# Optimization experiments

Hardware: AMD Instinct MI355X
Metric: run time of the kernel (lower is better)

Reference implementation:

```python
import jax, jax.numpy as jnp
import numpy as np

N, E, F, H, C = 100000, 3200000, 128, 256, 47
EPS = 1e-5


def setup_inputs() -> dict:
    key = jax.random.key(0)
    ks = jax.random.split(key, 12)
    x = jax.random.normal(ks[0], (N, F), dtype=jnp.float32)
    edge_index = jax.random.randint(ks[1], (2, E), 0, N, dtype=jnp.int64)
    relations = jax.random.randint(ks[2], (E,), 0, 4, dtype=jnp.int64)
    def lin(k, fan_in, fan_out):
        return jax.random.normal(k, (fan_in, fan_out), dtype=jnp.float32) / np.sqrt(fan_in)
    W0 = lin(ks[3], F, H); b0 = jnp.zeros((H,), jnp.float32)
    W1 = lin(ks[4], H, H); b1 = jnp.zeros((H,), jnp.float32)
    W2 = lin(ks[5], H, C); b2 = jnp.zeros((C,), jnp.float32)
    g0 = jnp.ones((H,), jnp.float32); be0 = jnp.zeros((H,), jnp.float32)
    g1 = jnp.ones((H,), jnp.float32); be1 = jnp.zeros((H,), jnp.float32)
    return {"x": x, "edge_index": edge_index, "relations": relations,
            "W0": W0, "b0": b0, "g0": g0, "be0": be0,
            "W1": W1, "b1": b1, "g1": g1, "be1": be1,
            "W2": W2, "b2": b2}


def _gcn_conv(x, W, b, src, dst, n_nodes):
    # GCNConv: linear transform, add self-loops, symmetric degree normalization,
    # gather-scale-scatter aggregation, bias add.
    h = x @ W  # [N, out]
    self_loop = jnp.arange(n_nodes, dtype=src.dtype)
    s = jnp.concatenate([src, self_loop])
    d = jnp.concatenate([dst, self_loop])
    deg = jax.ops.segment_sum(jnp.ones(d.shape[0], h.dtype), d, num_segments=n_nodes)
    dinv = jnp.where(deg > 0, jax.lax.rsqrt(deg), 0.0)
    coef = dinv[s] * dinv[d]  # [E+N]
    out = jax.ops.segment_sum(h[s] * coef[:, None], d, num_segments=n_nodes)
    return out + b


def _batch_norm(x, gamma, beta):
    mean = jnp.mean(x, axis=0)
    var = jnp.var(x, axis=0)
    return (x - mean) * jax.lax.rsqrt(var + EPS) * gamma + beta


def reference(x, edge_index, relations, W0, b0, g0, be0, W1, b1, g1, be1, W2, b2):
    src, dst = edge_index[0], edge_index[1]
    n = x.shape[0]
    h = _gcn_conv(x, W0, b0, src, dst, n)
    h = jax.nn.relu(_batch_norm(h, g0, be0))  # dropout is identity in eval
    h = _gcn_conv(h, W1, b1, src, dst, n)
    h = jax.nn.relu(_batch_norm(h, g1, be1))
    h = _gcn_conv(h, W2, b2, src, dst, n)
    return jax.nn.log_softmax(h, axis=-1)
```

## Files before the change

### kernel.cpp

```cpp
#include <hip/hip_runtime.h>
#include <hip/hip_fp8.h>
#include <math.h>

#define NN 100000
#define NE 3200000
#define FIN 128
#define HD 256
#define CO 47
#define NBKT 196
#define G 1024
#define CHUNK 3125

typedef _Float16 h2 __attribute__((ext_vector_type(2)));
typedef _Float16 h4 __attribute__((ext_vector_type(4)));
typedef _Float16 h8 __attribute__((ext_vector_type(8)));
typedef float f32x2 __attribute__((ext_vector_type(2)));
typedef float f32x4 __attribute__((ext_vector_type(4)));
typedef unsigned int u32x2 __attribute__((ext_vector_type(2)));
typedef unsigned int u32x4 __attribute__((ext_vector_type(4)));


__global__ __launch_bounds__(256) void hist_kernel(const int* __restrict__ dst,
                                                   int* __restrict__ hist) {
    __shared__ int h[NBKT];
    int tid = threadIdx.x;
    for (int i = tid; i < NBKT; i += 256) h[i] = 0;
    __syncthreads();
    int base = blockIdx.x * CHUNK;
    for (int i = tid; i < CHUNK; i += 256)
        atomicAdd(&h[dst[base + i] >> 9], 1);
    __syncthreads();
    for (int i = tid; i < NBKT; i += 256) hist[i * G + blockIdx.x] = h[i];
}

__global__ __launch_bounds__(256) void rowscan_kernel(int* __restrict__ hist,
                                                      int* __restrict__ btot) {
    __shared__ int sums[256];
    int b = blockIdx.x, t = threadIdx.x;
    int base = b * G + t * 4;
    int4 v = *(int4*)&hist[base];
    int i0 = v.x, i1 = i0 + v.y, i2 = i1 + v.z, i3 = i2 + v.w;
    sums[t] = i3;
    __syncthreads();
    #pragma unroll
    for (int off = 1; off < 256; off <<= 1) {
        int u = (t >= off) ? sums[t - off] : 0;
        __syncthreads();
        sums[t] += u;
        __syncthreads();
    }
    int excl = sums[t] - i3;
    hist[base] = excl;
    hist[base + 1] = excl + i0;
    hist[base + 2] = excl + i1;
    hist[base + 3] = excl + i2;
    if (t == 255) btot[b] = sums[255];
}

__global__ void totscan_kernel(const int* __restrict__ btot, int* __restrict__ bbase) {
    __shared__ int tmp[256];
    int t = threadIdx.x;
    int v = (t < NBKT) ? btot[t] : 0;
    tmp[t] = v;
    __syncthreads();
    #pragma unroll
    for (int off = 1; off < 256; off <<= 1) {
        int u = (t >= off) ? tmp[t - off] : 0;
        __syncthreads();
        tmp[t] += u;
        __syncthreads();
    }
    if (t < NBKT) bbase[t] = tmp[t] - v;
    if (t == NBKT - 1) bbase[NBKT] = tmp[t];
}

__global__ __launch_bounds__(256) void scatter_kernel(const int* __restrict__ src,
                                                      const int* __restrict__ dst,
                                                      const int* __restrict__ hscan,
                                                      const int* __restrict__ bbase,
                                                      int* __restrict__ epk) {
    __shared__ int cur[NBKT];
    int tid = threadIdx.x;
    for (int i = tid; i < NBKT; i += 256)
        cur[i] = hscan[i * G + blockIdx.x] + bbase[i];
    __syncthreads();
    int base = blockIdx.x * CHUNK;
    for (int i = tid; i < CHUNK; i += 256) {
        int e = base + i;
        int d = dst[e];
        int slot = atomicAdd(&cur[d >> 9], 1);
        epk[slot] = ((d & 511) << 17) | src[e];
    }
}

__global__ __launch_bounds__(256) void bucket_fill_kernel(
    const int* __restrict__ bbase, const int* __restrict__ epk,
    int* __restrict__ csr, int* __restrict__ offs, float* __restrict__ dinv)
{
    __shared__ int deg[512], cur[512], a0[512], a1[512];
    int tid = threadIdx.x, b = blockIdx.x;
    int ebeg = bbase[b], eend = bbase[b + 1];
    deg[tid] = 0; deg[tid + 256] = 0;
    __syncthreads();
    for (int e = ebeg + tid; e < eend; e += 256)
        atomicAdd(&deg[((unsigned)epk[e]) >> 17], 1);
    __syncthreads();
    a0[tid] = deg[tid]; a0[tid + 256] = deg[tid + 256];
    __syncthreads();
    int* pin = a0; int* pout = a1;
    for (int off = 1; off < 512; off <<= 1) {
        #pragma unroll
        for (int q = 0; q < 2; ++q) {
            int p = tid + q * 256;
            pout[p] = pin[p] + ((p >= off) ? pin[p - off] : 0);
        }
        __syncthreads();
        int* t = pin; pin = pout; pout = t;
    }
    #pragma unroll
    for (int q = 0; q < 2; ++q) {
        int i = tid + q * 256;
        int excl = pin[i] - deg[i];
        cur[i] = excl;
        int node = b * 512 + i;
        if (node < NN) {
            offs[node] = ebeg + excl;
            dinv[node] = rsqrtf((float)deg[i] + 1.0f);
        }
    }
    if (b == 0 && tid == 0) offs[NN] = NE;
    __syncthreads();
    for (int e = ebeg + tid; e < eend; e += 256) {
        int pk = epk[e];
        int p = atomicAdd(&cur[((unsigned)pk) >> 17], 1);
        csr[ebeg + p] = pk & 0x1FFFF;
    }
}


__global__ void wtrans_all_kernel(const float* __restrict__ W0,
                                  const float* __restrict__ W1,
                                  const float* __restrict__ W2,
                                  _Float16* __restrict__ wt0,
                                  _Float16* __restrict__ wt1,
                                  _Float16* __restrict__ wt2) {
    int i = blockIdx.x * 256 + threadIdx.x;
    if (i < 256 * 128) {
        int n = i >> 7, k = i & 127;
        wt0[i] = (_Float16)W0[k * 256 + n];
    } else if (i < 256 * 128 + 256 * 256) {
        int t = i - 256 * 128;
        int n = t >> 8, k = t & 255;
        wt1[t] = (_Float16)W1[k * 256 + n];
    } else if (i < 256 * 128 + 256 * 256 + 64 * 256) {
        int t = i - 256 * 128 - 256 * 256;
        int n = t >> 8, k = t & 255;
        wt2[t] = (_Float16)((n < CO) ? W2[k * CO + n] : 0.0f);
    }
}


__global__ void conv_x_kernel(const float* __restrict__ x, const float* __restrict__ dinv,
                              unsigned* __restrict__ xq) {
    int i = blockIdx.x * 256 + threadIdx.x;
    if (i >= NN * FIN / 4) return;
    int r = i >> 5;
    float4 v = ((const float4*)x)[i];
    float dv = dinv[r];
    int u = __builtin_amdgcn_cvt_pk_fp8_f32(v.x * dv, v.y * dv, 0, false);
    u = __builtin_amdgcn_cvt_pk_fp8_f32(v.z * dv, v.w * dv, u, true);
    xq[i] = (unsigned)u;
}


__global__ __launch_bounds__(256) void agg128_kernel(
    const unsigned* __restrict__ xq, const int* __restrict__ offs,
    const int* __restrict__ csr, const float* __restrict__ dinv,
    _Float16* __restrict__ out)
{
    int lane = threadIdx.x & 63;
    int grp = lane >> 5;
    int gl = lane & 31;
    int v = blockIdx.x * 4 + (threadIdx.x >> 6);
    f32x2 a01 = {0.f, 0.f}, a23 = {0.f, 0.f};
    if (grp == 0) {
        unsigned sv = xq[(size_t)v * 32 + gl];
        a01 += __builtin_amdgcn_cvt_pk_f32_fp8((int)sv, false);
        a23 += __builtin_amdgcn_cvt_pk_f32_fp8((int)sv, true);
    }
    int b = offs[v], e = offs[v + 1];
    int j = b + grp;
    int s[8];
    bool have = (j + 14 < e);
    if (have) {
        #pragma unroll
        for (int q = 0; q < 8; ++q) s[q] = csr[j + 2 * q];
    }
    while (have) {
        int nj = j + 16;
        bool nhave = (nj + 14 < e);
        int ns[8];
        if (nhave) {
            #pragma unroll
            for (int q = 0; q < 8; ++q) ns[q] = csr[nj + 2 * q];
        }
        #pragma unroll
        for (int q = 0; q < 8; ++q) {
            unsigned t = xq[(size_t)s[q] * 32 + gl];
            a01 += __builtin_amdgcn_cvt_pk_f32_fp8((int)t, false);
            a23 += __builtin_amdgcn_cvt_pk_f32_fp8((int)t, true);
        }
        #pragma unroll
        for (int q = 0; q < 8; ++q) s[q] = ns[q];
        j = nj; have = nhave;
    }
    for (; j < e; j += 2) {
        unsigned t = xq[(size_t)csr[j] * 32 + gl];
        a01 += __builtin_amdgcn_cvt_pk_f32_fp8((int)t, false);
        a23 += __builtin_amdgcn_cvt_pk_f32_fp8((int)t, true);
    }
    a01[0] += __shfl_xor(a01[0], 32, 64);
    a01[1] += __shfl_xor(a01[1], 32, 64);
    a23[0] += __shfl_xor(a23[0], 32, 64);
    a23[1] += __shfl_xor(a23[1], 32, 64);
    if (grp == 0) {
        float dv = dinv[v];
        h4 o; o[0] = (_Float16)(a01[0] * dv); o[1] = (_Float16)(a01[1] * dv);
        o[2] = (_Float16)(a23[0] * dv); o[3] = (_Float16)(a23[1] * dv);
        ((h4*)out)[(size_t)v * 32 + gl] = o;
    }
}

__global__ __launch_bounds__(256) void agg256_kernel(
    const unsigned* __restrict__ t1q, const int* __restrict__ offs,
    const int* __restrict__ csr, const float* __restrict__ dinv,
    unsigned* __restrict__ out)
{
    int lane = threadIdx.x & 63;
    int v = blockIdx.x * 4 + (threadIdx.x >> 6);
    unsigned sv = t1q[(size_t)v * 64 + lane];
    f32x2 acc01 = __builtin_amdgcn_cvt_pk_f32_fp8((int)sv, false);
    f32x2 acc23 = __builtin_amdgcn_cvt_pk_f32_fp8((int)sv, true);
    int b = offs[v], e = offs[v + 1], j = b;
    int s[8];
    if (j + 8 <= e) {
        #pragma unroll
        for (int q = 0; q < 8; ++q) s[q] = csr[j + q];
    }
    for (; j + 8 <= e; ) {
        int nj = j + 8;
        int ns[8];
        if (nj + 8 <= e) {
            #pragma unroll
            for (int q = 0; q < 8; ++q) ns[q] = csr[nj + q];
        }
        #pragma unroll
        for (int q = 0; q < 8; ++q) {
            unsigned t = t1q[(size_t)s[q] * 64 + lane];
            acc01 += __builtin_amdgcn_cvt_pk_f32_fp8((int)t, false);
            acc23 += __builtin_amdgcn_cvt_pk_f32_fp8((int)t, true);
        }
        #pragma unroll
        for (int q = 0; q < 8; ++q) s[q] = ns[q];
        j = nj;
    }
    for (; j < e; ++j) {
        unsigned t = t1q[(size_t)csr[j] * 64 + lane];
        acc01 += __builtin_amdgcn_cvt_pk_f32_fp8((int)t, false);
        acc23 += __builtin_amdgcn_cvt_pk_f32_fp8((int)t, true);
    }
    float dv = dinv[v];
    int pk = __builtin_amdgcn_cvt_pk_fp8_f32(acc01[0] * dv, acc01[1] * dv, 0, false);
    pk = __builtin_amdgcn_cvt_pk_fp8_f32(acc23[0] * dv, acc23[1] * dv, pk, true);
    out[(size_t)v * 64 + lane] = (unsigned)pk;
}

__global__ __launch_bounds__(256) void agg47_lsm_kernel(
    const unsigned* __restrict__ t2q, const int* __restrict__ offs,
    const int* __restrict__ csr, const float* __restrict__ dinv,
    const float* __restrict__ bias, float* __restrict__ out)
{
    int lane = threadIdx.x & 63;
    int grp = lane >> 4;
    int gl = lane & 15;
    int v = blockIdx.x * 4 + (threadIdx.x >> 6);
    f32x2 a01 = {0.f, 0.f}, a23 = {0.f, 0.f};
    if (grp == 0) {
        unsigned u = t2q[(size_t)v * 16 + gl];
        a01 += __builtin_amdgcn_cvt_pk_f32_fp8((int)u, false);
        a23 += __builtin_amdgcn_cvt_pk_f32_fp8((int)u, true);
    }
    int b = offs[v], e = offs[v + 1];
    int j = b + grp;
    int s[8];
    bool have = (j + 28 < e);
    if (have) {
        #pragma unroll
        for (int q = 0; q < 8; ++q) s[q] = csr[j + 4 * q];
    }
    while (have) {
        int nj = j + 32;
        bool nhave = (nj + 28 < e);
        int ns[8];
        if (nhave) {
            #pragma unroll
            for (int q = 0; q < 8; ++q) ns[q] = csr[nj + 4 * q];
        }
        #pragma unroll
        for (int q = 0; q < 8; ++q) {
            unsigned t = t2q[(size_t)s[q] * 16 + gl];
            a01 += __builtin_amdgcn_cvt_pk_f32_fp8((int)t, false);
            a23 += __builtin_amdgcn_cvt_pk_f32_fp8((int)t, true);
        }
        #pragma unroll
        for (int q = 0; q < 8; ++q) s[q] = ns[q];
        j = nj; have = nhave;
    }
    for (; j < e; j += 4) {
        unsigned t = t2q[(size_t)csr[j] * 16 + gl];
        a01 += __builtin_amdgcn_cvt_pk_f32_fp8((int)t, false);
        a23 += __builtin_amdgcn_cvt_pk_f32_fp8((int)t, true);
    }
    #pragma unroll
    for (int o = 16; o <= 32; o <<= 1) {
        a01[0] += __shfl_xor(a01[0], o, 64);
        a01[1] += __shfl_xor(a01[1], o, 64);
        a23[0] += __shfl_xor(a23[0], o, 64);
        a23[1] += __shfl_xor(a23[1], o, 64);
    }
    float dv = dinv[v];
    float vals[4] = {a01[0], a01[1], a23[0], a23[1]};
    float vv[4];
    #pragma unroll
    for (int k = 0; k < 4; ++k) {
        int c = 4 * gl + k;
        vv[k] = (c < CO) ? fmaf(vals[k], dv, bias[c]) : -1e30f;
    }
    float m = fmaxf(fmaxf(vv[0], vv[1]), fmaxf(vv[2], vv[3]));
    #pragma unroll
    for (int o = 8; o > 0; o >>= 1) m = fmaxf(m, __shfl_xor(m, o, 64));
    float sum = 0.f;
    #pragma unroll
    for (int k = 0; k < 4; ++k) sum += (vv[k] > -1e29f) ? expf(vv[k] - m) : 0.f;
    #pragma unroll
    for (int o = 8; o > 0; o >>= 1) sum += __shfl_xor(sum, o, 64);
    float lse = m + logf(sum);
    if (grp == 0) {
        #pragma unroll
        for (int k = 0; k < 4; ++k) {
            int c = 4 * gl + k;
            if (c < CO) out[(size_t)v * CO + c] = vv[k] - lse;
        }
    }
}


#define LDS_PAD 8

template<int K, bool XFORM, bool EPI_DINV, bool OUT8, bool BNSTAT>
__global__ __launch_bounds__(256) void mfma_gemm_big(
    const _Float16* __restrict__ A, int lda,
    const _Float16* __restrict__ Wt,
    const float* __restrict__ ss, const float* __restrict__ dinv,
    void* __restrict__ outp, int ldo, float* __restrict__ part8)
{
    __shared__ __align__(16) _Float16 As[128][64 + LDS_PAD];
    __shared__ __align__(16) _Float16 Bs[128][64 + LDS_PAD];
    __shared__ float SS[2 * K];
    __shared__ float cstat[256];
    const int row0 = (blockIdx.x >> 1) * 128;
    const int col0 = (blockIdx.x & 1) * 128;
    const int tid = threadIdx.x;
    if (XFORM) {
        for (int i = tid; i < 2 * K; i += 256) SS[i] = ss[i];
    }
    if (BNSTAT) cstat[tid] = 0.f;
    const int lane = tid & 63;
    const int wv = tid >> 6;
    const int wr = wv >> 1, wc = wv & 1;
    const int fr = lane & 15;
    const int kb = (lane >> 4) * 8;

    f32x4 acc[4][4];
    #pragma unroll
    for (int m = 0; m < 4; ++m)
        #pragma unroll
        for (int n = 0; n < 4; ++n)
            acc[m][n] = (f32x4){0.f, 0.f, 0.f, 0.f};

    if (XFORM || BNSTAT) __syncthreads();

    for (int k0 = 0; k0 < K; k0 += 64) {
        #pragma unroll
        for (int p = 0; p < 4; ++p) {
            int c = p * 256 + tid;
            int m = c >> 3, kk = (c & 7) * 8;
            int r = row0 + m;
            h8 av = {};
            if (r < NN) av = *(const h8*)&A[(size_t)r * lda + k0 + kk];
            if (XFORM) {
                #pragma unroll
                for (int j = 0; j < 8; ++j) {
                    float a = (float)av[j];
                    a = fmaxf(fmaf(a, SS[k0 + kk + j], SS[K + k0 + kk + j]), 0.0f);
                    av[j] = (_Float16)a;
                }
            }
            *(h8*)&As[m][kk] = av;
        }
        #pragma unroll
        for (int p = 0; p < 4; ++p) {
            int c = p * 256 + tid;
            int n = c >> 3, kk = (c & 7) * 8;
            h8 bv = *(const h8*)&Wt[(size_t)(col0 + n) * K + k0 + kk];
            *(h8*)&Bs[n][kk] = bv;
        }
        __syncthreads();
        #pragma unroll
        for (int ks = 0; ks < 2; ++ks) {
            h8 a[4], b[4];
            #pragma unroll
            for (int m = 0; m < 4; ++m)
                a[m] = *(const h8*)&As[wr * 64 + m * 16 + fr][ks * 32 + kb];
            #pragma unroll
            for (int n = 0; n < 4; ++n)
                b[n] = *(const h8*)&Bs[wc * 64 + n * 16 + fr][ks * 32 + kb];
            #pragma unroll
            for (int m = 0; m < 4; ++m)
                #pragma unroll
                for (int n = 0; n < 4; ++n)
                    acc[m][n] = __builtin_amdgcn_mfma_f32_16x16x32_f16(a[m], b[n], acc[m][n], 0, 0, 0);
        }
        __syncthreads();
    }

    const int fq = lane >> 4;
    if (OUT8) {
        unsigned char* stg = (unsigned char*)&As[0][0];
        #pragma unroll
        for (int m = 0; m < 4; ++m) {
            #pragma unroll
            for (int j = 0; j < 4; ++j) {
                int rr = wr * 64 + m * 16 + fq * 4 + j;
                int r = row0 + rr;
                float dv = (EPI_DINV && r < NN) ? dinv[r] : 1.0f;
                #pragma unroll
                for (int n = 0; n < 4; n += 2) {
                    int cc0 = wc * 64 + n * 16 + fr;
                    float v0 = acc[m][n][j] * dv;
                    float v1 = acc[m][n + 1][j] * dv;
                    int pk = __builtin_amdgcn_cvt_pk_fp8_f32(v0, v1, 0, false);
                    stg[rr * 128 + cc0] = (unsigned char)(pk & 0xFF);
                    stg[rr * 128 + cc0 + 16] = (unsigned char)((pk >> 8) & 0xFF);
                }
            }
        }
        __syncthreads();
        #pragma unroll
        for (int p = 0; p < 4; ++p) {
            int rr = p * 32 + (tid >> 3);
            int cc = (tid & 7) * 16;
            int r = row0 + rr;
            if (r < NN)
                *(u32x4*)&((unsigned char*)outp)[(size_t)r * ldo + col0 + cc] =
                    *(u32x4*)&stg[rr * 128 + cc];
        }
    } else {
        float ps[4] = {}, pq[4] = {};
        #pragma unroll
        for (int m = 0; m < 4; ++m) {
            #pragma unroll
            for (int j = 0; j < 4; ++j) {
                int r = row0 + wr * 64 + m * 16 + fq * 4 + j;
                if (r >= NN) continue;
                float dv = EPI_DINV ? dinv[r] : 1.0f;
                #pragma unroll
                for (int n = 0; n < 4; ++n) {
                    int c = col0 + wc * 64 + n * 16 + fr;
                    float val = acc[m][n][j] * dv;
                    ((_Float16*)outp)[(size_t)r * ldo + c] = (_Float16)val;
                    if (BNSTAT) { ps[n] += val; pq[n] += val * val; }
                }
            }
        }
        if (BNSTAT) {
            #pragma unroll
            for (int n = 0; n < 4; ++n) {
                int cc = wc * 64 + n * 16 + fr;
                atomicAdd(&cstat[cc], ps[n]);
                atomicAdd(&cstat[128 + cc], pq[n]);
            }
            __syncthreads();
            if (tid < 128) {
                int rep = (blockIdx.x & 7) * 512;
                atomicAdd(&part8[rep + col0 + tid], cstat[tid]);
                atomicAdd(&part8[rep + 256 + col0 + tid], cstat[128 + tid]);
            }
        }
    }
}


__global__ __launch_bounds__(256) void mfma_gemm2_kernel(
    const unsigned* __restrict__ Aq,
    const _Float16* __restrict__ Wt,
    const float* __restrict__ ss, const float* __restrict__ dinv,
    unsigned char* __restrict__ t2q)
{
    __shared__ __align__(16) _Float16 As[128][32 + LDS_PAD];
    __shared__ __align__(16) _Float16 Bs[64][32 + LDS_PAD];
    __shared__ float SS[2 * HD];
    const int row0 = blockIdx.x * 128;
    const int tid = threadIdx.x;
    for (int i = tid; i < 2 * HD; i += 256) SS[i] = ss[i];
    const int lane = tid & 63;
    const int wv = tid >> 6;
    const int wr = wv >> 1, wc = wv & 1;
    const int fr = lane & 15;
    const int kb = (lane >> 4) * 8;

    f32x4 acc[4][2];
    #pragma unroll
    for (int m = 0; m < 4; ++m)
        #pragma unroll
        for (int n = 0; n < 2; ++n)
            acc[m][n] = (f32x4){0.f, 0.f, 0.f, 0.f};

    __syncthreads();

    for (int k0 = 0; k0 < HD; k0 += 32) {
        #pragma unroll
        for (int p = 0; p < 2; ++p) {
            int idx = (p * 256 + tid) * 8;
            int m = idx >> 5, kk = idx & 31;
            int r = row0 + m;
            float vals[8] = {};
            if (r < NN) {
                u32x2 u = *(const u32x2*)&Aq[(size_t)r * 64 + ((k0 + kk) >> 2)];
                f32x2 p0 = __builtin_amdgcn_cvt_pk_f32_fp8((int)u[0], false);
                f32x2 p1 = __builtin_amdgcn_cvt_pk_f32_fp8((int)u[0], true);
                f32x2 p2 = __builtin_amdgcn_cvt_pk_f32_fp8((int)u[1], false);
                f32x2 p3 = __builtin_amdgcn_cvt_pk_f32_fp8((int)u[1], true);
                vals[0] = p0[0]; vals[1] = p0[1]; vals[2] = p1[0]; vals[3] = p1[1];
                vals[4] = p2[0]; vals[5] = p2[1]; vals[6] = p3[0]; vals[7] = p3[1];
            }
            h8 av;
            #pragma unroll
            for (int j = 0; j < 8; ++j) {
                float a = fmaxf(fmaf(vals[j], SS[k0 + kk + j], SS[HD + k0 + kk + j]), 0.0f);
                av[j] = (_Float16)a;
            }
            *(h8*)&As[m][kk] = av;
        }
        {
            int idx = tid * 8;
            int n = idx >> 5, kk = idx & 31;
            h8 bv = *(const h8*)&Wt[(size_t)n * HD + k0 + kk];
            *(h8*)&Bs[n][kk] = bv;
        }
        __syncthreads();
        h8 a[4], b[2];
        #pragma unroll
        for (int m = 0; m < 4; ++m)
            a[m] = *(const h8*)&As[wr * 64 + m * 16 + fr][kb];
        #pragma unroll
        for (int n = 0; n < 2; ++n)
            b[n] = *(const h8*)&Bs[wc * 32 + n * 16 + fr][kb];
        #pragma unroll
        for (int m = 0; m < 4; ++m)
            #pragma unroll
            for (int n = 0; n < 2; ++n)
                acc[m][n] = __builtin_amdgcn_mfma_f32_16x16x32_f16(a[m], b[n], acc[m][n], 0, 0, 0);
        __syncthreads();
    }

    const int fq = lane >> 4;
    unsigned char* stg = (unsigned char*)&As[0][0];
    #pragma unroll
    for (int m = 0; m < 4; ++m) {
        #pragma unroll
        for (int j = 0; j < 4; ++j) {
            int rr = wr * 64 + m * 16 + fq * 4 + j;
            int r = row0 + rr;
            float dv = (r < NN) ? dinv[r] : 1.0f;
            int cc0 = wc * 32 + fr;
            float v0 = acc[m][0][j] * dv;
            float v1 = acc[m][1][j] * dv;
            int pk = __builtin_amdgcn_cvt_pk_fp8_f32(v0, v1, 0, false);
            stg[rr * 64 + cc0] = (unsigned char)(pk & 0xFF);
            stg[rr * 64 + cc0 + 16] = (unsigned char)((pk >> 8) & 0xFF);
        }
    }
    __syncthreads();
    #pragma unroll
    for (int p = 0; p < 2; ++p) {
        int idx = p * 256 + tid;
        int rr = idx >> 2;
        int cc = (idx & 3) * 16;
        int r = row0 + rr;
        if (r < NN)
            *(u32x4*)&t2q[(size_t)r * 64 + cc] = *(u32x4*)&stg[rr * 64 + cc];
    }
}


__global__ void bn_finalize8_kernel(const float* __restrict__ part8,
                                    const float* __restrict__ g,
                                    const float* __restrict__ be,
                                    float* __restrict__ ss) {
    int t = threadIdx.x;
    float s1 = 0.f, s2 = 0.f;
    #pragma unroll
    for (int x = 0; x < 8; ++x) {
        s1 += part8[x * 512 + t];
        s2 += part8[x * 512 + 256 + t];
    }
    float mean = s1 * (1.0f / NN);
    float var = s2 * (1.0f / NN) - mean * mean;
    float sc = g[t] * rsqrtf(var + 1e-5f);
    ss[t] = sc;
    ss[HD + t] = be[t] - mean * sc;
}

__global__ __launch_bounds__(256) void bn_part8_kernel(const unsigned* __restrict__ h,
                                                       float* __restrict__ part) {
    int tid = threadIdx.x;
    int fg = tid & 63;
    int rg = tid >> 6;
    float s1[4] = {}, s2[4] = {};
    for (int r = blockIdx.x * 4 + rg; r < NN; r += 4096) {
        unsigned u = h[(size_t)r * 64 + fg];
        f32x2 a = __builtin_amdgcn_cvt_pk_f32_fp8((int)u, false);
        f32x2 b = __builtin_amdgcn_cvt_pk_f32_fp8((int)u, true);
        float f0 = a[0], f1 = a[1], f2 = b[0], f3 = b[1];
        s1[0] += f0; s2[0] += f0 * f0;
        s1[1] += f1; s2[1] += f1 * f1;
        s1[2] += f2; s2[2] += f2 * f2;
        s1[3] += f3; s2[3] += f3 * f3;
    }
    __shared__ float sm[256][8];
    #pragma unroll
    for (int j = 0; j < 4; ++j) { sm[tid][j] = s1[j]; sm[tid][4 + j] = s2[j]; }
    __syncthreads();
    if (tid < 64) {
        float o1[4] = {}, o2[4] = {};
        #pragma unroll
        for (int r = 0; r < 4; ++r)
            #pragma unroll
            for (int j = 0; j < 4; ++j) {
                o1[j] += sm[r * 64 + tid][j];
                o2[j] += sm[r * 64 + tid][4 + j];
            }
        #pragma unroll
        for (int j = 0; j < 4; ++j) {
            part[(size_t)blockIdx.x * 512 + tid * 4 + j] = o1[j];
            part[(size_t)blockIdx.x * 512 + 256 + tid * 4 + j] = o2[j];
        }
    }
}

__global__ __launch_bounds__(256) void bn_reduce_kernel(const float* __restrict__ part,
                                                        const float* __restrict__ g,
                                                        const float* __restrict__ be,
                                                        float* __restrict__ ss) {
    int f = blockIdx.x * 32 + (threadIdx.x & 31);
    int c = threadIdx.x >> 5;
    float s1 = 0.f, s2 = 0.f;
    for (int b = c; b < 1024; b += 8) {
        s1 += part[(size_t)b * 512 + f];
        s2 += part[(size_t)b * 512 + 256 + f];
    }
    __shared__ float m1[8][32], m2[8][32];
    m1[c][threadIdx.x & 31] = s1; m2[c][threadIdx.x & 31] = s2;
    __syncthreads();
    if (threadIdx.x < 32) {
        float t1 = 0.f, t2 = 0.f;
        #pragma unroll
        for (int q = 0; q < 8; ++q) { t1 += m1[q][threadIdx.x]; t2 += m2[q][threadIdx.x]; }
        float mean = t1 * (1.0f / NN);
        float var = t2 * (1.0f / NN) - mean * mean;
        float sc = g[f] * rsqrtf(var + 1e-5f);
        ss[f] = sc;
        ss[HD + f] = be[f] - mean * sc;
    }
}


extern "C" void kernel_launch(void* const* d_in, const int* in_sizes, int n_in,
                              void* d_out, int out_size, void* d_ws, size_t ws_size,
                              hipStream_t stream) {
    const float* x   = (const float*)d_in[0];
    const int*   ei  = (const int*)d_in[1];
    const float* W0  = (const float*)d_in[3];
    const float* g0  = (const float*)d_in[5];
    const float* be0 = (const float*)d_in[6];
    const float* W1  = (const float*)d_in[7];
    const float* g1  = (const float*)d_in[9];
    const float* be1 = (const float*)d_in[10];
    const float* W2  = (const float*)d_in[11];
    const float* b2  = (const float*)d_in[12];
    float* out = (float*)d_out;

    const int* src = ei;
    const int* dst = ei + NE;

    const size_t S = 51200000;
    char* ws = (char*)d_ws;
    unsigned*       xq  = (unsigned*)ws;
    unsigned*       t1q = (unsigned*)ws;
    unsigned char*  t2q = (unsigned char*)ws;
    _Float16*       a0  = (_Float16*)(ws + 25600000);
    _Float16*       S2  = (_Float16*)(ws + S);
    unsigned*       h1q = (unsigned*)(ws + S);
    char* base2 = ws + 2 * S;
    int*   csr  = (int*)  (base2);
    int*   offs = (int*)  (base2 + 12800000);
    float* dinv = (float*)(base2 + 13200064);
    float* ssb  = (float*)(base2 + 13602112);
    int*   btot = (int*)  (base2 + 13604160);
    int*   bbase= (int*)  (base2 + 13605184);
    _Float16* wt0 = (_Float16*)(base2 + 13608320);
    _Float16* wt1 = (_Float16*)(base2 + 13673856);
    _Float16* wt2 = (_Float16*)(base2 + 13804928);
    int*   hist = (int*)  (base2 + 13837696);
    int*   epk  = (int*)  (base2 + 14640576);
    float* part = (float*)(base2 + 27440576);
    float* part8= (float*)(base2 + 29537728);

    hist_kernel<<<G, 256, 0, stream>>>(dst, hist);
    rowscan_kernel<<<NBKT, 256, 0, stream>>>(hist, btot);
    totscan_kernel<<<1, 256, 0, stream>>>(btot, bbase);
    scatter_kernel<<<G, 256, 0, stream>>>(src, dst, hist, bbase, epk);
    bucket_fill_kernel<<<NBKT, 256, 0, stream>>>(bbase, epk, csr, offs, dinv);

    wtrans_all_kernel<<<448, 256, 0, stream>>>(W0, W1, W2, wt0, wt1, wt2);

    const int MB = (NN + 127) / 128;

    hipMemsetAsync(part8, 0, 8 * 512 * sizeof(float), stream);
    conv_x_kernel<<<(NN * FIN / 4 + 255) / 256, 256, 0, stream>>>(x, dinv, xq);
    agg128_kernel<<<NN / 4, 256, 0, stream>>>(xq, offs, csr, dinv, a0);
    mfma_gemm_big<FIN, false, false, false, true><<<MB * 2, 256, 0, stream>>>(
        a0, FIN, wt0, nullptr, dinv, S2, HD, part8);
    bn_finalize8_kernel<<<1, HD, 0, stream>>>(part8, g0, be0, ssb);

    mfma_gemm_big<HD, true, true, true, false><<<MB * 2, 256, 0, stream>>>(
        S2, HD, wt1, ssb, dinv, t1q, HD, nullptr);
    agg256_kernel<<<NN / 4, 256, 0, stream>>>(t1q, offs, csr, dinv, h1q);

    bn_part8_kernel<<<1024, 256, 0, stream>>>(h1q, part);
    bn_reduce_kernel<<<8, 256, 0, stream>>>(part, g1, be1, ssb);

    mfma_gemm2_kernel<<<MB, 256, 0, stream>>>(h1q, wt2, ssb, dinv, t2q);
    agg47_lsm_kernel<<<NN / 4, 256, 0, stream>>>((const unsigned*)t2q, offs, csr, dinv, b2, out);
}
```

Before: 545.8 us.

## Widen GEMM tiles to full 256 columns and use 4-way edge split in agg128

```diff
diff --git a/kernel.cpp b/kernel.cpp
--- a/kernel.cpp
+++ b/kernel.cpp
@@ -179,55 +179,68 @@
     _Float16* __restrict__ out)
 {
     int lane = threadIdx.x & 63;
-    int grp = lane >> 5;
-    int gl = lane & 31;
+    int grp = lane >> 4;
+    int gl = lane & 15;
     int v = blockIdx.x * 4 + (threadIdx.x >> 6);
-    f32x2 a01 = {0.f, 0.f}, a23 = {0.f, 0.f};
+    const u32x2* rows = (const u32x2*)xq;
+    f32x2 c0 = {0.f, 0.f}, c1 = {0.f, 0.f}, c2 = {0.f, 0.f}, c3 = {0.f, 0.f};
     if (grp == 0) {
-        unsigned sv = xq[(size_t)v * 32 + gl];
-        a01 += __builtin_amdgcn_cvt_pk_f32_fp8((int)sv, false);
-        a23 += __builtin_amdgcn_cvt_pk_f32_fp8((int)sv, true);
+        u32x2 u = rows[(size_t)v * 16 + gl];
+        c0 += __builtin_amdgcn_cvt_pk_f32_fp8((int)u[0], false);
+        c1 += __builtin_amdgcn_cvt_pk_f32_fp8((int)u[0], true);
+        c2 += __builtin_amdgcn_cvt_pk_f32_fp8((int)u[1], false);
+        c3 += __builtin_amdgcn_cvt_pk_f32_fp8((int)u[1], true);
     }
     int b = offs[v], e = offs[v + 1];
     int j = b + grp;
     int s[8];
-    bool have = (j + 14 < e);
+    bool have = (j + 28 < e);
     if (have) {
         #pragma unroll
-        for (int q = 0; q < 8; ++q) s[q] = csr[j + 2 * q];
+        for (int q = 0; q < 8; ++q) s[q] = csr[j + 4 * q];
     }
     while (have) {
-        int nj = j + 16;
-        bool nhave = (nj + 14 < e);
+        int nj = j + 32;
+        bool nhave = (nj + 28 < e);
         int ns[8];
         if (nhave) {
             #pragma unroll
-            for (int q = 0; q < 8; ++q) ns[q] = csr[nj + 2 * q];
+            for (int q = 0; q < 8; ++q) ns[q] = csr[nj + 4 * q];
         }
         #pragma unroll
         for (int q = 0; q < 8; ++q) {
-            unsigned t = xq[(size_t)s[q] * 32 + gl];
-            a01 += __builtin_amdgcn_cvt_pk_f32_fp8((int)t, false);
-            a23 += __builtin_amdgcn_cvt_pk_f32_fp8((int)t, true);
+            u32x2 t = rows[(size_t)s[q] * 16 + gl];
+            c0 += __builtin_amdgcn_cvt_pk_f32_fp8((int)t[0], false);
+            c1 += __builtin_amdgcn_cvt_pk_f32_fp8((int)t[0], true);
+            c2 += __builtin_amdgcn_cvt_pk_f32_fp8((int)t[1], false);
+            c3 += __builtin_amdgcn_cvt_pk_f32_fp8((int)t[1], true);
         }
         #pragma unroll
         for (int q = 0; q < 8; ++q) s[q] = ns[q];
         j = nj; have = nhave;
     }
-    for (; j < e; j += 2) {
-        unsigned t = xq[(size_t)csr[j] * 32 + gl];
-        a01 += __builtin_amdgcn_cvt_pk_f32_fp8((int)t, false);
-        a23 += __builtin_amdgcn_cvt_pk_f32_fp8((int)t, true);
-    }
-    a01[0] += __shfl_xor(a01[0], 32, 64);
-    a01[1] += __shfl_xor(a01[1], 32, 64);
-    a23[0] += __shfl_xor(a23[0], 32, 64);
-    a23[1] += __shfl_xor(a23[1], 32, 64);
+    for (; j < e; j += 4) {
+        u32x2 t = rows[(size_t)csr[j] * 16 + gl];
+        c0 += __builtin_amdgcn_cvt_pk_f32_fp8((int)t[0], false);
+        c1 += __builtin_amdgcn_cvt_pk_f32_fp8((int)t[0], true);
+        c2 += __builtin_amdgcn_cvt_pk_f32_fp8((int)t[1], false);
+        c3 += __builtin_amdgcn_cvt_pk_f32_fp8((int)t[1], true);
+    }
+    #pragma unroll
+    for (int o = 16; o <= 32; o <<= 1) {
+        c0[0] += __shfl_xor(c0[0], o, 64); c0[1] += __shfl_xor(c0[1], o, 64);
+        c1[0] += __shfl_xor(c1[0], o, 64); c1[1] += __shfl_xor(c1[1], o, 64);
+        c2[0] += __shfl_xor(c2[0], o, 64); c2[1] += __shfl_xor(c2[1], o, 64);
+        c3[0] += __shfl_xor(c3[0], o, 64); c3[1] += __shfl_xor(c3[1], o, 64);
+    }
     if (grp == 0) {
         float dv = dinv[v];
-        h4 o; o[0] = (_Float16)(a01[0] * dv); o[1] = (_Float16)(a01[1] * dv);
-        o[2] = (_Float16)(a23[0] * dv); o[3] = (_Float16)(a23[1] * dv);
-        ((h4*)out)[(size_t)v * 32 + gl] = o;
+        h8 o8;
+        o8[0] = (_Float16)(c0[0] * dv); o8[1] = (_Float16)(c0[1] * dv);
+        o8[2] = (_Float16)(c1[0] * dv); o8[3] = (_Float16)(c1[1] * dv);
+        o8[4] = (_Float16)(c2[0] * dv); o8[5] = (_Float16)(c2[1] * dv);
+        o8[6] = (_Float16)(c3[0] * dv); o8[7] = (_Float16)(c3[1] * dv);
+        ((h8*)out)[(size_t)v * 16 + gl] = o8;
     }
 }
 
@@ -358,34 +371,33 @@
 #define LDS_PAD 8
 
 template<int K, bool XFORM, bool EPI_DINV, bool OUT8, bool BNSTAT>
-__global__ __launch_bounds__(256) void mfma_gemm_big(
+__global__ __launch_bounds__(256) void mfma_gemm_wide(
     const _Float16* __restrict__ A, int lda,
     const _Float16* __restrict__ Wt,
     const float* __restrict__ ss, const float* __restrict__ dinv,
     void* __restrict__ outp, int ldo, float* __restrict__ part8)
 {
     __shared__ __align__(16) _Float16 As[128][64 + LDS_PAD];
-    __shared__ __align__(16) _Float16 Bs[128][64 + LDS_PAD];
+    __shared__ __align__(16) _Float16 Bs[256][64 + LDS_PAD];
     __shared__ float SS[2 * K];
-    __shared__ float cstat[256];
-    const int row0 = (blockIdx.x >> 1) * 128;
-    const int col0 = (blockIdx.x & 1) * 128;
+    __shared__ float cstat[512];
+    const int row0 = blockIdx.x * 128;
     const int tid = threadIdx.x;
     if (XFORM) {
         for (int i = tid; i < 2 * K; i += 256) SS[i] = ss[i];
     }
-    if (BNSTAT) cstat[tid] = 0.f;
+    if (BNSTAT) { cstat[tid] = 0.f; cstat[tid + 256] = 0.f; }
     const int lane = tid & 63;
     const int wv = tid >> 6;
     const int wr = wv >> 1, wc = wv & 1;
     const int fr = lane & 15;
     const int kb = (lane >> 4) * 8;
 
-    f32x4 acc[4][4];
+    f32x4 acc[4][8];
     #pragma unroll
     for (int m = 0; m < 4; ++m)
         #pragma unroll
-        for (int n = 0; n < 4; ++n)
+        for (int n = 0; n < 8; ++n)
             acc[m][n] = (f32x4){0.f, 0.f, 0.f, 0.f};
 
     if (XFORM || BNSTAT) __syncthreads();
@@ -409,26 +421,26 @@
             *(h8*)&As[m][kk] = av;
         }
         #pragma unroll
-        for (int p = 0; p < 4; ++p) {
+        for (int p = 0; p < 8; ++p) {
             int c = p * 256 + tid;
             int n = c >> 3, kk = (c & 7) * 8;
-            h8 bv = *(const h8*)&Wt[(size_t)(col0 + n) * K + k0 + kk];
+            h8 bv = *(const h8*)&Wt[(size_t)n * K + k0 + kk];
             *(h8*)&Bs[n][kk] = bv;
         }
         __syncthreads();
         #pragma unroll
         for (int ks = 0; ks < 2; ++ks) {
-            h8 a[4], b[4];
+            h8 a[4], b[8];
             #pragma unroll
             for (int m = 0; m < 4; ++m)
                 a[m] = *(const h8*)&As[wr * 64 + m * 16 + fr][ks * 32 + kb];
             #pragma unroll
-            for (int n = 0; n < 4; ++n)
-                b[n] = *(const h8*)&Bs[wc * 64 + n * 16 + fr][ks * 32 + kb];
+            for (int n = 0; n < 8; ++n)
+                b[n] = *(const h8*)&Bs[wc * 128 + n * 16 + fr][ks * 32 + kb];
             #pragma unroll
             for (int m = 0; m < 4; ++m)
                 #pragma unroll
-                for (int n = 0; n < 4; ++n)
+                for (int n = 0; n < 8; ++n)
                     acc[m][n] = __builtin_amdgcn_mfma_f32_16x16x32_f16(a[m], b[n], acc[m][n], 0, 0, 0);
         }
         __syncthreads();
@@ -436,7 +448,7 @@
 
     const int fq = lane >> 4;
     if (OUT8) {
-        unsigned char* stg = (unsigned char*)&As[0][0];
+        unsigned char* stg = (unsigned char*)&Bs[0][0];
         #pragma unroll
         for (int m = 0; m < 4; ++m) {
             #pragma unroll
@@ -445,28 +457,29 @@
                 int r = row0 + rr;
                 float dv = (EPI_DINV && r < NN) ? dinv[r] : 1.0f;
                 #pragma unroll
-                for (int n = 0; n < 4; n += 2) {
-                    int cc0 = wc * 64 + n * 16 + fr;
+                for (int n = 0; n < 8; n += 2) {
+                    int cc0 = wc * 128 + n * 16 + fr;
                     float v0 = acc[m][n][j] * dv;
                     float v1 = acc[m][n + 1][j] * dv;
                     int pk = __builtin_amdgcn_cvt_pk_fp8_f32(v0, v1, 0, false);
-                    stg[rr * 128 + cc0] = (unsigned char)(pk & 0xFF);
-                    stg[rr * 128 + cc0 + 16] = (unsigned char)((pk >> 8) & 0xFF);
+                    stg[rr * 256 + cc0] = (unsigned char)(pk & 0xFF);
+                    stg[rr * 256 + cc0 + 16] = (unsigned char)((pk >> 8) & 0xFF);
                 }
             }
         }
         __syncthreads();
         #pragma unroll
-        for (int p = 0; p < 4; ++p) {
-            int rr = p * 32 + (tid >> 3);
-            int cc = (tid & 7) * 16;
+        for (int p = 0; p < 8; ++p) {
+            int idx = p * 256 + tid;
+            int rr = idx >> 4;
+            int cc = (idx & 15) * 16;
             int r = row0 + rr;
             if (r < NN)
-                *(u32x4*)&((unsigned char*)outp)[(size_t)r * ldo + col0 + cc] =
-                    *(u32x4*)&stg[rr * 128 + cc];
+                *(u32x4*)&((unsigned char*)outp)[(size_t)r * ldo + cc] =
+                    *(u32x4*)&stg[rr * 256 + cc];
         }
     } else {
-        float ps[4] = {}, pq[4] = {};
+        float ps[8] = {}, pq[8] = {};
         #pragma unroll
         for (int m = 0; m < 4; ++m) {
             #pragma unroll
@@ -475,8 +488,8 @@
                 if (r >= NN) continue;
                 float dv = EPI_DINV ? dinv[r] : 1.0f;
                 #pragma unroll
-                for (int n = 0; n < 4; ++n) {
-                    int c = col0 + wc * 64 + n * 16 + fr;
+                for (int n = 0; n < 8; ++n) {
+                    int c = wc * 128 + n * 16 + fr;
                     float val = acc[m][n][j] * dv;
                     ((_Float16*)outp)[(size_t)r * ldo + c] = (_Float16)val;
                     if (BNSTAT) { ps[n] += val; pq[n] += val * val; }
@@ -485,17 +498,15 @@
         }
         if (BNSTAT) {
             #pragma unroll
-            for (int n = 0; n < 4; ++n) {
-                int cc = wc * 64 + n * 16 + fr;
+            for (int n = 0; n < 8; ++n) {
+                int cc = wc * 128 + n * 16 + fr;
                 atomicAdd(&cstat[cc], ps[n]);
-                atomicAdd(&cstat[128 + cc], pq[n]);
+                atomicAdd(&cstat[256 + cc], pq[n]);
             }
             __syncthreads();
-            if (tid < 128) {
-                int rep = (blockIdx.x & 7) * 512;
-                atomicAdd(&part8[rep + col0 + tid], cstat[tid]);
-                atomicAdd(&part8[rep + 256 + col0 + tid], cstat[128 + tid]);
-            }
+            int rep = (blockIdx.x & 7) * 512;
+            atomicAdd(&part8[rep + tid], cstat[tid]);
+            atomicAdd(&part8[rep + 256 + tid], cstat[256 + tid]);
         }
     }
 }
@@ -740,11 +751,11 @@
     hipMemsetAsync(part8, 0, 8 * 512 * sizeof(float), stream);
     conv_x_kernel<<<(NN * FIN / 4 + 255) / 256, 256, 0, stream>>>(x, dinv, xq);
     agg128_kernel<<<NN / 4, 256, 0, stream>>>(xq, offs, csr, dinv, a0);
-    mfma_gemm_big<FIN, false, false, false, true><<<MB * 2, 256, 0, stream>>>(
+    mfma_gemm_wide<FIN, false, false, false, true><<<MB, 256, 0, stream>>>(
         a0, FIN, wt0, nullptr, dinv, S2, HD, part8);
     bn_finalize8_kernel<<<1, HD, 0, stream>>>(part8, g0, be0, ssb);
 
-    mfma_gemm_big<HD, true, true, true, false><<<MB * 2, 256, 0, stream>>>(
+    mfma_gemm_wide<HD, true, true, true, false><<<MB, 256, 0, stream>>>(
         S2, HD, wt1, ssb, dinv, t1q, HD, nullptr);
     agg256_kernel<<<NN / 4, 256, 0, stream>>>(t1q, offs, csr, dinv, h1q);
 
```

After: 595.9 us. +9.2%, slower.
